# Optimization experiments

Hardware: AMD Instinct MI355X
Metric: run time of the kernel (lower is better)

## Reference

```python
import jax, jax.numpy as jnp
import numpy as np

SIGMA = 4.0  # PIL ImageFilter.GaussianBlur(radius=4) ~ Gaussian with sigma=4
HALF = int(3 * SIGMA)  # truncate at 3 sigma -> 25-tap kernel


def _gauss_1d():
    x = np.arange(-HALF, HALF + 1, dtype=np.float32)
    k = np.exp(-0.5 * (x / SIGMA) ** 2)
    return jnp.asarray(k / k.sum())


def setup_inputs() -> dict:
    key = jax.random.key(0)
    img = jax.random.uniform(key, (1, 3, 4096, 4096), dtype=jnp.float32)
    return {"img": img}


def reference(img):
    # map_max = img.max(); blur(img[0]/map_max) * map_max  (PIL Gaussian blur)
    k = _gauss_1d()  # [25]
    ksz = k.shape[0]
    map_max = img.max()
    x = img[0] / map_max                      # [C, H, W]
    C = x.shape[0]
    x = x[None]                               # [1, C, H, W]
    # PIL extends edges when blurring -> replicate padding
    x = jnp.pad(x, ((0, 0), (0, 0), (HALF, HALF), (HALF, HALF)), mode='edge')
    dn = ('NCHW', 'OIHW', 'NCHW')
    kh = jnp.broadcast_to(k.reshape(1, 1, ksz, 1), (C, 1, ksz, 1))
    kw = jnp.broadcast_to(k.reshape(1, 1, 1, ksz), (C, 1, 1, ksz))
    # separable depthwise Gaussian: vertical then horizontal pass
    x = jax.lax.conv_general_dilated(x, kh, (1, 1), 'VALID',
                                     feature_group_count=C, dimension_numbers=dn)
    x = jax.lax.conv_general_dilated(x, kw, (1, 1), 'VALID',
                                     feature_group_count=C, dimension_numbers=dn)
    return x[0] * map_max                     # [C, H, W]
```

## Files before the change

kernel.cpp:

```cpp
#include <hip/hip_runtime.h>
#include <hip/hip_bf16.h>


#define IMG_W 4096
#define IMG_H 4096
#define N_CH  3
#define HALF  12
#define KSZ   25

#define TILE_W 96
#define TILE_H 32
#define COLS   (TILE_W + 2*HALF)
#define LDS_STRIDE 124
#define GRP_ROWS 8
#define N_GRP    4
#define VROWS (GRP_ROWS + 2*HALF)
#define VCOLS2 (COLS/2)
#define HCHUNK 12
#define HPAIRS (HCHUNK/2)
#define HREAD  (HCHUNK + 2*HALF)

typedef float f2 __attribute__((ext_vector_type(2)));
typedef float f4 __attribute__((ext_vector_type(4)));

__device__ __constant__ float kW[KSZ] = {
    0.00110988f, 0.00227883f, 0.00438965f, 0.00794860f, 0.01352109f,
    0.02160664f, 0.03243540f, 0.04574124f, 0.06059730f, 0.07541456f,
    0.08816855f, 0.09683420f, 0.09990806f, 0.09683420f, 0.08816855f,
    0.07541456f, 0.06059730f, 0.04574124f, 0.03243540f, 0.02160664f,
    0.01352109f, 0.00794860f, 0.00438965f, 0.00227883f, 0.00110988f
};

__device__ __constant__ f2 kW2[26] = {
    {0.00110988f, 0.f},
    {0.00227883f, 0.00110988f},
    {0.00438965f, 0.00227883f},
    {0.00794860f, 0.00438965f},
    {0.01352109f, 0.00794860f},
    {0.02160664f, 0.01352109f},
    {0.03243540f, 0.02160664f},
    {0.04574124f, 0.03243540f},
    {0.06059730f, 0.04574124f},
    {0.07541456f, 0.06059730f},
    {0.08816855f, 0.07541456f},
    {0.09683420f, 0.08816855f},
    {0.09990806f, 0.09683420f},
    {0.09683420f, 0.09990806f},
    {0.08816855f, 0.09683420f},
    {0.07541456f, 0.08816855f},
    {0.06059730f, 0.07541456f},
    {0.04574124f, 0.06059730f},
    {0.03243540f, 0.04574124f},
    {0.02160664f, 0.03243540f},
    {0.01352109f, 0.02160664f},
    {0.00794860f, 0.01352109f},
    {0.00438965f, 0.00794860f},
    {0.00227883f, 0.00438965f},
    {0.00110988f, 0.00227883f},
    {0.f,         0.00110988f}
};

__global__ __launch_bounds__(256)
void gauss_blur_fused(const float* __restrict__ img, float* __restrict__ out)
{
    __shared__ float inter[TILE_H * LDS_STRIDE];

    const int tid = threadIdx.x;
    const int x0  = blockIdx.x * TILE_W;
    const int y0  = blockIdx.y * TILE_H;
    const int c   = blockIdx.z;

    const float* __restrict__ src = img + (size_t)c * IMG_W * IMG_H;
    float* __restrict__ dst       = out + (size_t)c * IMG_W * IMG_H;

    if (tid < VCOLS2 * N_GRP) {
        const int c2 = tid % VCOLS2;
        const int g  = tid / VCOLS2;
        const int gx = x0 - HALF + 2 * c2;
        const int ybase = y0 + g * GRP_ROWS - HALF;
        const int ldscol = 2 * c2;

        f2 w[VROWS];

        if (gx >= 0 && gx <= IMG_W - 2) {
            if (ybase >= 0 && ybase + VROWS <= IMG_H) {
                const float* p = src + (size_t)ybase * IMG_W + gx;
                #pragma unroll
                for (int j = 0; j < VROWS; ++j)
                    w[j] = *(const f2*)(p + (size_t)j * IMG_W);
            } else {
                #pragma unroll
                for (int j = 0; j < VROWS; ++j) {
                    int gy = ybase + j;
                    gy = gy < 0 ? 0 : (gy > IMG_H - 1 ? IMG_H - 1 : gy);
                    w[j] = *(const f2*)(src + (size_t)gy * IMG_W + gx);
                }
            }
        } else {
            const int gc = gx < 0 ? 0 : IMG_W - 1;
            #pragma unroll
            for (int j = 0; j < VROWS; ++j) {
                int gy = ybase + j;
                gy = gy < 0 ? 0 : (gy > IMG_H - 1 ? IMG_H - 1 : gy);
                const float v = src[(size_t)gy * IMG_W + gc];
                w[j].x = v; w[j].y = v;
            }
        }

        #pragma unroll
        for (int i = 0; i < GRP_ROWS; ++i) {
            f2 a = (f2)(0.f);
            #pragma unroll
            for (int k = 0; k < KSZ; ++k)
                a += kW[k] * w[i + k];
            *(f2*)&inter[(g * GRP_ROWS + i) * LDS_STRIDE + ldscol] = a;
        }
    }
    __syncthreads();

    {
        const int row   = tid >> 3;
        const int chunk = tid & 7;
        const int xl    = chunk * HCHUNK;

        f4 t[HREAD / 4];
        const f4* lp = (const f4*)&inter[row * LDS_STRIDE + xl];
        #pragma unroll
        for (int m4 = 0; m4 < HREAD / 4; ++m4)
            t[m4] = lp[m4];

        f2 acc2[HPAIRS];
        #pragma unroll
        for (int p = 0; p < HPAIRS; ++p) acc2[p] = (f2)(0.f);

        #pragma unroll
        for (int m4 = 0; m4 < HREAD / 4; ++m4) {
            #pragma unroll
            for (int e = 0; e < 4; ++e) {
                const int m = 4 * m4 + e;
                const float wv = t[m4][e];
                const int pmin = (m >= 25) ? (m - 24) / 2 : 0;
                const int pmax = (m / 2) < (HPAIRS - 1) ? (m / 2) : (HPAIRS - 1);
                #pragma unroll
                for (int p = pmin; p <= pmax; ++p)
                    acc2[p] += wv * kW2[m - 2 * p];
            }
        }

        const size_t rowbase = (size_t)(y0 + row) * IMG_W;
        const int gx0 = x0 + xl;
        #pragma unroll
        for (int j4 = 0; j4 < HCHUNK / 4; ++j4) {
            f4 o;
            o.x = acc2[2 * j4 + 0].x; o.y = acc2[2 * j4 + 0].y;
            o.z = acc2[2 * j4 + 1].x; o.w = acc2[2 * j4 + 1].y;
            const int gx = gx0 + 4 * j4;
            if (gx < IMG_W)
                *(f4*)&dst[rowbase + gx] = o;
        }
    }
}

extern "C" void kernel_launch(void* const* d_in, const int* in_sizes, int n_in,
                              void* d_out, int out_size, void* d_ws, size_t ws_size,
                              hipStream_t stream)
{
    const float* img = (const float*)d_in[0];
    float* out = (float*)d_out;

    dim3 grid((IMG_W + TILE_W - 1) / TILE_W,
              IMG_H / TILE_H,
              N_CH);
    dim3 block(256);
    gauss_blur_fused<<<grid, block, 0, stream>>>(img, out);
}
```

Baseline: 387.5 us.

## Stage interior input tiles into LDS via direct global_load_lds before vertical pass

For interior tiles, the whole (TILE_H+24)x120 input halo region is copied into shared memory with 16-byte global_load_lds instructions spread across all 256 threads. The vertical pass then reads its column pairs from LDS instead of issuing strided 8-byte global loads from only 240 threads. Boundary tiles keep the old clamped global-load path. The intent is wider, coalesced loads that use every thread, at the cost of about 27KB of extra LDS per block, which may lower occupancy, plus an extra barrier.

After: 344.2 us. 11.2% less time.

```diff
diff --git a/kernel.cpp b/kernel.cpp
--- a/kernel.cpp
+++ b/kernel.cpp
@@ -20,8 +20,16 @@
 #define HPAIRS (HCHUNK/2)
 #define HREAD  (HCHUNK + 2*HALF)
 
+#define IN_ROWS   (TILE_H + 2*HALF)
+#define IN_FLAT   (IN_ROWS * COLS)
+#define IN_CHUNKS 27
+#define IN_PAD    (IN_CHUNKS * 256)
+
 typedef float f2 __attribute__((ext_vector_type(2)));
 typedef float f4 __attribute__((ext_vector_type(4)));
+
+typedef const __attribute__((address_space(1))) void gas_t;
+typedef __attribute__((address_space(3))) void las_t;
 
 __device__ __constant__ float kW[KSZ] = {
     0.00110988f, 0.00227883f, 0.00438965f, 0.00794860f, 0.01352109f,
@@ -63,57 +71,104 @@
 __global__ __launch_bounds__(256)
 void gauss_blur_fused(const float* __restrict__ img, float* __restrict__ out)
 {
+    __shared__ float in_lds[IN_PAD];
     __shared__ float inter[TILE_H * LDS_STRIDE];
 
     const int tid = threadIdx.x;
-    const int x0  = blockIdx.x * TILE_W;
-    const int y0  = blockIdx.y * TILE_H;
+    const int bx  = blockIdx.x;
+    const int ty  = blockIdx.y;
+    const int x0  = bx * TILE_W;
+    const int y0  = ty * TILE_H;
     const int c   = blockIdx.z;
 
     const float* __restrict__ src = img + (size_t)c * IMG_W * IMG_H;
     float* __restrict__ dst       = out + (size_t)c * IMG_W * IMG_H;
 
-    if (tid < VCOLS2 * N_GRP) {
-        const int c2 = tid % VCOLS2;
-        const int g  = tid / VCOLS2;
-        const int gx = x0 - HALF + 2 * c2;
-        const int ybase = y0 + g * GRP_ROWS - HALF;
-        const int ldscol = 2 * c2;
-
-        f2 w[VROWS];
-
-        if (gx >= 0 && gx <= IMG_W - 2) {
-            if (ybase >= 0 && ybase + VROWS <= IMG_H) {
-                const float* p = src + (size_t)ybase * IMG_W + gx;
-                #pragma unroll
-                for (int j = 0; j < VROWS; ++j)
-                    w[j] = *(const f2*)(p + (size_t)j * IMG_W);
+    const bool interior = (bx >= 1) && (bx <= 41) && (ty >= 1) && (ty <= 126);
+
+    if (interior) {
+        const int w    = tid >> 6;
+        const int lane = tid & 63;
+        const float* gbase = src + (size_t)(y0 - HALF) * IMG_W + (x0 - HALF);
+        #pragma unroll
+        for (int k = 0; k < 7; ++k) {
+            const int chunk = 4 * k + w;
+            if (chunk < IN_CHUNKS) {
+                int fo = chunk * 256 + lane * 4;
+                fo = fo > (IN_FLAT - 4) ? (IN_FLAT - 4) : fo;
+                const int r   = fo / COLS;
+                const int col = fo - r * COLS;
+                __builtin_amdgcn_global_load_lds(
+                    (gas_t*)(gbase + (size_t)r * IMG_W + col),
+                    (las_t*)&in_lds[chunk * 256],
+                    16, 0, 0);
+            }
+        }
+        __syncthreads();
+
+        if (tid < VCOLS2 * N_GRP) {
+            const int c2 = tid % VCOLS2;
+            const int g  = tid / VCOLS2;
+            const int ldscol = 2 * c2;
+            const float* ip = &in_lds[g * GRP_ROWS * COLS + 2 * c2];
+
+            f2 wrow[VROWS];
+            #pragma unroll
+            for (int j = 0; j < VROWS; ++j)
+                wrow[j] = *(const f2*)(ip + j * COLS);
+
+            #pragma unroll
+            for (int i = 0; i < GRP_ROWS; ++i) {
+                f2 a = (f2)(0.f);
+                #pragma unroll
+                for (int k = 0; k < KSZ; ++k)
+                    a += kW[k] * wrow[i + k];
+                *(f2*)&inter[(g * GRP_ROWS + i) * LDS_STRIDE + ldscol] = a;
+            }
+        }
+    } else {
+        if (tid < VCOLS2 * N_GRP) {
+            const int c2 = tid % VCOLS2;
+            const int g  = tid / VCOLS2;
+            const int gx = x0 - HALF + 2 * c2;
+            const int ybase = y0 + g * GRP_ROWS - HALF;
+            const int ldscol = 2 * c2;
+
+            f2 wrow[VROWS];
+
+            if (gx >= 0 && gx <= IMG_W - 2) {
+                if (ybase >= 0 && ybase + VROWS <= IMG_H) {
+                    const float* p = src + (size_t)ybase * IMG_W + gx;
+                    #pragma unroll
+                    for (int j = 0; j < VROWS; ++j)
+                        wrow[j] = *(const f2*)(p + (size_t)j * IMG_W);
+                } else {
+                    #pragma unroll
+                    for (int j = 0; j < VROWS; ++j) {
+                        int gy = ybase + j;
+                        gy = gy < 0 ? 0 : (gy > IMG_H - 1 ? IMG_H - 1 : gy);
+                        wrow[j] = *(const f2*)(src + (size_t)gy * IMG_W + gx);
+                    }
+                }
             } else {
+                const int gc = gx < 0 ? 0 : IMG_W - 1;
                 #pragma unroll
                 for (int j = 0; j < VROWS; ++j) {
                     int gy = ybase + j;
                     gy = gy < 0 ? 0 : (gy > IMG_H - 1 ? IMG_H - 1 : gy);
-                    w[j] = *(const f2*)(src + (size_t)gy * IMG_W + gx);
+                    const float v = src[(size_t)gy * IMG_W + gc];
+                    wrow[j].x = v; wrow[j].y = v;
                 }
             }
-        } else {
-            const int gc = gx < 0 ? 0 : IMG_W - 1;
-            #pragma unroll
-            for (int j = 0; j < VROWS; ++j) {
-                int gy = ybase + j;
-                gy = gy < 0 ? 0 : (gy > IMG_H - 1 ? IMG_H - 1 : gy);
-                const float v = src[(size_t)gy * IMG_W + gc];
-                w[j].x = v; w[j].y = v;
-            }
-        }
-
-        #pragma unroll
-        for (int i = 0; i < GRP_ROWS; ++i) {
-            f2 a = (f2)(0.f);
-            #pragma unroll
-            for (int k = 0; k < KSZ; ++k)
-                a += kW[k] * w[i + k];
-            *(f2*)&inter[(g * GRP_ROWS + i) * LDS_STRIDE + ldscol] = a;
+
+            #pragma unroll
+            for (int i = 0; i < GRP_ROWS; ++i) {
+                f2 a = (f2)(0.f);
+                #pragma unroll
+                for (int k = 0; k < KSZ; ++k)
+                    a += kW[k] * wrow[i + k];
+                *(f2*)&inter[(g * GRP_ROWS + i) * LDS_STRIDE + ldscol] = a;
+            }
         }
     }
     __syncthreads();
```
